# Kernel tuning notes

Hardware: AMD Instinct MI355X
Metric: run time of the kernel (lower is better)

Reference implementation:

```python
import jax, jax.numpy as jnp
import numpy as np

D_MODEL = 1024
N_HEADS = 16
HEAD_DIM = D_MODEL // N_HEADS  # 64
GRID = 8  # 8x8 Ising grid over head_dim pixels
N_DIFF_STEPS = 2
STEPS_PER_SAMPLE = 8  # cfg sampling.steps_per_sample
BETA_START = 0.8
BETA_END = 1.2


def setup_inputs() -> dict:
    key = jax.random.key(0)
    k1, k2, k3 = jax.random.split(key, 3)
    B, N = 4, 4096
    q = jax.random.normal(k1, (B, N, D_MODEL), dtype=jnp.float32)
    k = jax.random.normal(k2, (B, N, D_MODEL), dtype=jnp.float32)
    v = jax.random.normal(k3, (B, N, D_MODEL), dtype=jnp.float32)
    return {"q": q, "k": k, "v": v}


def _nbr_field(s):
    # s: (..., G, G) spins in {-1, +1}; 4-neighbor sum with open (non-torus) boundary
    zr = jnp.zeros_like(s[..., :1, :])
    zc = jnp.zeros_like(s[..., :, :1])
    up = jnp.concatenate([s[..., 1:, :], zr], axis=-2)
    down = jnp.concatenate([zr, s[..., :-1, :]], axis=-2)
    left = jnp.concatenate([s[..., :, 1:], zc], axis=-1)
    right = jnp.concatenate([zc, s[..., :, :-1]], axis=-1)
    return up + down + left + right


def _fta_forward(v):
    B, N, D = v.shape
    H, HD = N_HEADS, HEAD_DIM
    # binarize values -> Ising spins per head: (B, H, N, G, G)
    vh = v.reshape(B, N, H, HD).transpose(0, 2, 1, 3)
    spins = jnp.where(vh > 0, 1.0, -1.0).astype(jnp.float32).reshape(B, H, N, GRID, GRID)

    # log-spaced beta schedule (diffusion_schedule kind='log'), each diffusion
    # step runs STEPS_PER_SAMPLE Gibbs sweeps
    betas = jnp.exp(jnp.linspace(jnp.log(BETA_START), jnp.log(BETA_END), N_DIFF_STEPS))
    betas = jnp.repeat(betas, STEPS_PER_SAMPLE)  # (T,)
    T = N_DIFF_STEPS * STEPS_PER_SAMPLE

    ii, jj = jnp.meshgrid(jnp.arange(GRID), jnp.arange(GRID), indexing="ij")
    parity = ((ii + jj) % 2).astype(jnp.float32)  # checkerboard mask (G, G)

    keys = jax.random.split(jax.random.key(1234), T)

    def gibbs_step(s, xs):
        beta, kk = xs
        k0, k1 = jax.random.split(kk)

        def half_sweep(s, mask, kh):
            h = _nbr_field(s)
            p = jax.nn.sigmoid(2.0 * beta * h)  # P(spin=+1 | neighbors)
            u = jax.random.uniform(kh, s.shape, dtype=s.dtype)
            new = jnp.where(u < p, 1.0, -1.0)
            return jnp.where(mask > 0.5, new, s)

        s = half_sweep(s, parity, k0)
        s = half_sweep(s, 1.0 - parity, k1)
        return s, None

    spins, _ = jax.lax.scan(gibbs_step, spins, (betas, keys))

    # back to (B, N, D); spins already in {-1, +1} == bool*2-1
    out = spins.reshape(B, H, N, HD).transpose(0, 2, 1, 3).reshape(B, N, D)
    return out


def reference(q, k, v):
    # q and k are accepted for interface fidelity but, as in the source
    # module's head_fta, only v participates in the computation.
    return _fta_forward(v)
```

## Files before the change

kernel.cpp:

```cpp
#include <hip/hip_runtime.h>
#include <stdint.h>
#include <string.h>
#include <math.h>


struct FtaParams {
  uint32_t hk[32][2];
  uint32_t K9[2][9];
};

static inline void tf2x32_host(uint32_t k0, uint32_t k1, uint32_t c0, uint32_t c1,
                               uint32_t& o0, uint32_t& o1) {
  uint32_t ks2 = k0 ^ k1 ^ 0x1BD11BDAu;
  uint32_t x0 = c0 + k0, x1 = c1 + k1;
#define TFR(r) { x0 += x1; x1 = (x1 << (r)) | (x1 >> (32 - (r))); x1 ^= x0; }
  TFR(13) TFR(15) TFR(26) TFR(6)
  x0 += k1;  x1 += ks2 + 1u;
  TFR(17) TFR(29) TFR(16) TFR(24)
  x0 += ks2; x1 += k0 + 2u;
  TFR(13) TFR(15) TFR(26) TFR(6)
  x0 += k0;  x1 += k1 + 3u;
  TFR(17) TFR(29) TFR(16) TFR(24)
  x0 += k1;  x1 += ks2 + 4u;
  TFR(13) TFR(15) TFR(26) TFR(6)
  x0 += ks2; x1 += k0 + 5u;
#undef TFR
  o0 = x0; o1 = x1;
}

__device__ __forceinline__ static void tf_bits4(
    uint32_t K0, uint32_t K1, uint32_t ks2,
    uint32_t i1, uint32_t i2, uint32_t i3, uint32_t i4, uint32_t i5,
    uint32_t m0, uint32_t m1, uint32_t m2, uint32_t m3,
    uint32_t& o0, uint32_t& o1, uint32_t& o2, uint32_t& o3) {
#define ROTL(x, r) __builtin_amdgcn_alignbit((x), (x), 32u - (r))
#define QR4(r)                                                             \
  a0 += a1; b0 += b1; c0 += c1; d0 += d1;                                  \
  a1 = ROTL(a1, r) ^ a0; b1 = ROTL(b1, r) ^ b0;                            \
  c1 = ROTL(c1, r) ^ c0; d1 = ROTL(d1, r) ^ d0;
#define INJ4(sx, si)                                                       \
  a0 += sx; b0 += sx; c0 += sx; d0 += sx;                                  \
  a1 += si; b1 += si; c1 += si; d1 += si;
  uint32_t a1 = m0, b1 = m1, c1 = m2, d1 = m3;
  uint32_t a0 = K0 + a1, b0 = K0 + b1, c0 = K0 + c1, d0 = K0 + d1;
  a1 = ROTL(a1, 13) ^ a0; b1 = ROTL(b1, 13) ^ b0;
  c1 = ROTL(c1, 13) ^ c0; d1 = ROTL(d1, 13) ^ d0;
  QR4(15) QR4(26) QR4(6)
  INJ4(K1, i1)
  QR4(17) QR4(29) QR4(16) QR4(24)
  INJ4(ks2, i2)
  QR4(13) QR4(15) QR4(26) QR4(6)
  INJ4(K0, i3)
  QR4(17) QR4(29) QR4(16) QR4(24)
  INJ4(K1, i4)
  QR4(13) QR4(15) QR4(26) QR4(6)
  a0 += ks2; b0 += ks2; c0 += ks2; d0 += ks2;
  a1 += i5;  b1 += i5;  c1 += i5;  d1 += i5;
  o0 = a0 ^ a1; o1 = b0 ^ b1; o2 = c0 ^ c1; o3 = d0 ^ d1;
#undef QR4
#undef INJ4
#undef ROTL
}

__global__ __launch_bounds__(256, 4) void fta_kernel(const float* __restrict__ v,
                                                     float* __restrict__ out,
                                                     FtaParams P) {
  uint32_t tid = blockIdx.x * 256u + threadIdx.x;
  uint32_t b = tid >> 16;
  uint32_t h = (tid >> 12) & 15u;
  uint32_t n = tid & 4095u;

  size_t voff = ((size_t)(b * 4096u + n)) * 1024u + (size_t)h * 64u;

  uint64_t bd = 0;
#pragma unroll
  for (int k = 0; k < 64; k += 4) {
    float4 a = *reinterpret_cast<const float4*>(v + voff + k);
    bd |= ((uint64_t)(a.x > 0.0f)) << (k + 0);
    bd |= ((uint64_t)(a.y > 0.0f)) << (k + 1);
    bd |= ((uint64_t)(a.z > 0.0f)) << (k + 2);
    bd |= ((uint64_t)(a.w > 0.0f)) << (k + 3);
  }

  uint32_t mbase = tid * 64u;

  uint32_t K[9];
#pragma unroll
  for (int q = 0; q < 9; ++q) K[q] = P.K9[0][q];

  const uint64_t PMASK[2] = { 0x55AA55AA55AA55AAull, 0xAA55AA55AA55AA55ull };

  for (int t = 0; t < 16; ++t) {
    if (t == 8) {
#pragma unroll
      for (int q = 0; q < 9; ++q) K[q] = P.K9[1][q];
    }
#pragma unroll
    for (int hf = 0; hf < 2; ++hf) {
      const uint32_t K0 = P.hk[2 * t + hf][0];
      const uint32_t K1 = P.hk[2 * t + hf][1];
      const uint32_t ks2 = K0 ^ K1 ^ 0x1BD11BDAu;
      const uint32_t i1 = ks2 + 1u, i2 = K0 + 2u, i3 = K1 + 3u,
                     i4 = ks2 + 4u, i5 = K0 + 5u;

      uint64_t U = bd >> 8;
      uint64_t D = bd << 8;
      uint64_t L = (bd >> 1) & 0x7f7f7f7f7f7f7f7full;
      uint64_t R = (bd << 1) & 0xfefefefefefefefeull;
      uint64_t t0 = U ^ D, ca = U & D;
      uint64_t t1 = L ^ R, cb = L & R;
      uint64_t c0 = t0 ^ t1, cc = t0 & t1;
      uint64_t cx = ca ^ cb;
      uint64_t c1 = cx ^ cc;
      uint64_t c2 = (ca & cb) | (cc & cx);

      uint32_t accLo = 0u, accHi = 0u;
#pragma unroll
      for (int i = 0; i < 8; ++i) {
        const int j0 = (i + 1 + hf) & 1;
        const int kr = i * 8 + j0;
        uint32_t bits[4];
        tf_bits4(K0, K1, ks2, i1, i2, i3, i4, i5,
                 mbase + (K1 + (uint32_t)(kr + 0)),
                 mbase + (K1 + (uint32_t)(kr + 2)),
                 mbase + (K1 + (uint32_t)(kr + 4)),
                 mbase + (K1 + (uint32_t)(kr + 6)),
                 bits[0], bits[1], bits[2], bits[3]);
#pragma unroll
        for (int jj = 0; jj < 4; ++jj) {
          const int j = 2 * jj + j0;
          const int k = i * 8 + j;
          uint32_t b0 = (uint32_t)(c0 >> k) & 1u;
          uint32_t b1 = (uint32_t)(c1 >> k) & 1u;
          const int e = (int)(i == 0) + (int)(i == 7) + (int)(j == 0) + (int)(j == 7);
          uint32_t thr;
          if (e == 0) {
            uint32_t b2 = (uint32_t)(c2 >> k) & 1u;
            uint32_t tA = b0 ? K[2] : K[0];
            uint32_t tB = b0 ? K[6] : K[4];
            uint32_t tC = b1 ? tB : tA;
            thr = b2 ? K[8] : tC;
          } else if (e == 1) {
            uint32_t tA = b0 ? K[3] : K[1];
            uint32_t tB = b0 ? K[7] : K[5];
            thr = b1 ? tB : tA;
          } else {
            uint32_t tA = b0 ? K[4] : K[2];
            thr = b1 ? K[6] : tA;
          }

          uint32_t nb = (bits[jj] < thr) ? 1u : 0u;
          if (k < 32) accLo |= nb << k;
          else        accHi |= nb << (k - 32);
        }
      }
      uint64_t acc = ((uint64_t)accHi << 32) | (uint64_t)accLo;
      bd = (bd & ~PMASK[hf]) | acc;
    }
  }

#pragma unroll
  for (int k = 0; k < 64; k += 4) {
    float4 o;
    o.x = ((bd >> (k + 0)) & 1ull) ? 1.0f : -1.0f;
    o.y = ((bd >> (k + 1)) & 1ull) ? 1.0f : -1.0f;
    o.z = ((bd >> (k + 2)) & 1ull) ? 1.0f : -1.0f;
    o.w = ((bd >> (k + 3)) & 1ull) ? 1.0f : -1.0f;
    *reinterpret_cast<float4*>(out + voff + k) = o;
  }
}

static float xla_expf(float xin) {
  const float exp_hi = 88.3762626647950f;
  const float exp_lo = -88.3762626647949f;
  const float LOG2EF = 1.44269504088896341f;
  const float C1 = 0.693359375f;
  const float C2 = -2.12194440e-4f;
  const float Pc0 = 1.9875691500E-4f;
  const float Pc1 = 1.3981999507E-3f;
  const float Pc2 = 8.3334519073E-3f;
  const float Pc3 = 4.1665795894E-2f;
  const float Pc4 = 1.6666665459E-1f;
  const float Pc5 = 5.0000001201E-1f;
#define MA(a, b, c) ((a) * (b) + (c))
  float x = xin;
  if (x > exp_hi) x = exp_hi;
  if (x < exp_lo) x = exp_lo;
  float fx = floorf(MA(x, LOG2EF, 0.5f));
  float tmp = C1 * fx;
  float z = C2 * fx;
  x = x - tmp;
  x = x - z;
  z = x * x;
  float y = MA(x, Pc0, Pc1);
  y = MA(y, x, Pc2);
  y = MA(y, x, Pc3);
  y = MA(y, x, Pc4);
  y = MA(y, x, Pc5);
  y = MA(y, z, x);
  y = y + 1.0f;
  int nn = (int)fx;
  uint32_t eb = (uint32_t)(nn + 127) << 23;
  float p2n;
  memcpy(&p2n, &eb, 4);
  float r = y * p2n;
  return r > xin ? r : xin;
#undef MA
}

extern "C" void kernel_launch(void* const* d_in, const int* in_sizes, int n_in,
                              void* d_out, int out_size, void* d_ws, size_t ws_size,
                              hipStream_t stream) {
  (void)in_sizes; (void)n_in; (void)d_ws; (void)ws_size; (void)out_size;
  const float* v = (const float*)d_in[2];
  float* out = (float*)d_out;

  FtaParams P;

  const uint32_t rk0 = 0u, rk1 = 1234u;
  uint32_t kt[16][2];
  for (uint32_t t = 0; t < 16; ++t) tf2x32_host(rk0, rk1, 0u, t, kt[t][0], kt[t][1]);
  for (int t = 0; t < 16; ++t) {
    uint32_t a0, a1, b0, b1;
    tf2x32_host(kt[t][0], kt[t][1], 0u, 0u, a0, a1);
    tf2x32_host(kt[t][0], kt[t][1], 0u, 1u, b0, b1);
    P.hk[2 * t + 0][0] = a0; P.hk[2 * t + 0][1] = a1;
    P.hk[2 * t + 1][0] = b0; P.hk[2 * t + 1][1] = b1;
  }

  float bet[2];
  bet[0] = (float)exp((double)(float)log((double)0.8f));
  bet[1] = (float)exp((double)(float)log((double)1.2f));

  for (int s = 0; s < 2; ++s) {
    float x2b = 2.0f * bet[s];
    for (int hh = -4; hh <= 4; ++hh) {
      float xh = x2b * (float)hh;
      float e = xla_expf(-xh);
      float p = 1.0f / (1.0f + e);
      double pd = (double)p * 8388608.0;
      uint64_t kc = (uint64_t)ceil(pd);
      uint64_t k9 = kc << 9;
      P.K9[s][hh + 4] = (k9 > 0xFFFFFFFFull) ? 0xFFFFFFFFu : (uint32_t)k9;
    }
  }

  fta_kernel<<<dim3(1024), dim3(256), 0, stream>>>(v, out, P);
}
```

Before: 537.4 us.

## Split each 8x8 Ising grid across two lanes exchanging boundary rows via shuffle

```diff
diff --git a/kernel.cpp b/kernel.cpp
--- a/kernel.cpp
+++ b/kernel.cpp
@@ -62,33 +62,39 @@
 #undef ROTL
 }
 
-__global__ __launch_bounds__(256, 4) void fta_kernel(const float* __restrict__ v,
+__global__ __launch_bounds__(256, 8) void fta_kernel(const float* __restrict__ v,
                                                      float* __restrict__ out,
                                                      FtaParams P) {
   uint32_t tid = blockIdx.x * 256u + threadIdx.x;
-  uint32_t b = tid >> 16;
-  uint32_t h = (tid >> 12) & 15u;
-  uint32_t n = tid & 4095u;
-
-  size_t voff = ((size_t)(b * 4096u + n)) * 1024u + (size_t)h * 64u;
-
-  uint64_t bd = 0;
-#pragma unroll
-  for (int k = 0; k < 64; k += 4) {
+  const int half = (int)(tid & 1u);
+  uint32_t g = tid >> 1;
+  uint32_t b = g >> 16;
+  uint32_t h = (g >> 12) & 15u;
+  uint32_t n = g & 4095u;
+
+  size_t voff = ((size_t)(b * 4096u + n)) * 1024u + (size_t)h * 64u
+              + (size_t)(half * 32);
+
+  uint32_t nat = 0u;
+#pragma unroll
+  for (int k = 0; k < 32; k += 4) {
     float4 a = *reinterpret_cast<const float4*>(v + voff + k);
-    bd |= ((uint64_t)(a.x > 0.0f)) << (k + 0);
-    bd |= ((uint64_t)(a.y > 0.0f)) << (k + 1);
-    bd |= ((uint64_t)(a.z > 0.0f)) << (k + 2);
-    bd |= ((uint64_t)(a.w > 0.0f)) << (k + 3);
-  }
-
-  uint32_t mbase = tid * 64u;
+    nat |= ((uint32_t)(a.x > 0.0f)) << (k + 0);
+    nat |= ((uint32_t)(a.y > 0.0f)) << (k + 1);
+    nat |= ((uint32_t)(a.z > 0.0f)) << (k + 2);
+    nat |= ((uint32_t)(a.w > 0.0f)) << (k + 3);
+  }
+  uint32_t bd = half ? __brev(nat) : nat;
+
+  const uint32_t mgrid = g * 64u;
+  const uint32_t mpc = mgrid + (half ? 63u : 0u);
+  const int sgn = half ? -1 : 1;
 
   uint32_t K[9];
 #pragma unroll
   for (int q = 0; q < 9; ++q) K[q] = P.K9[0][q];
 
-  const uint64_t PMASK[2] = { 0x55AA55AA55AA55AAull, 0xAA55AA55AA55AA55ull };
+  const uint32_t PM[2] = { 0x55AA55AAu, 0xAA55AA55u };
 
   for (int t = 0; t < 16; ++t) {
     if (t == 8) {
@@ -102,70 +108,73 @@
       const uint32_t ks2 = K0 ^ K1 ^ 0x1BD11BDAu;
       const uint32_t i1 = ks2 + 1u, i2 = K0 + 2u, i3 = K1 + 3u,
                      i4 = ks2 + 4u, i5 = K0 + 5u;
-
-      uint64_t U = bd >> 8;
-      uint64_t D = bd << 8;
-      uint64_t L = (bd >> 1) & 0x7f7f7f7f7f7f7f7full;
-      uint64_t R = (bd << 1) & 0xfefefefefefefefeull;
-      uint64_t t0 = U ^ D, ca = U & D;
-      uint64_t t1 = L ^ R, cb = L & R;
-      uint64_t c0 = t0 ^ t1, cc = t0 & t1;
-      uint64_t cx = ca ^ cb;
-      uint64_t c1 = cx ^ cc;
-      uint64_t c2 = (ca & cb) | (cc & cx);
-
-      uint32_t accLo = 0u, accHi = 0u;
-#pragma unroll
-      for (int i = 0; i < 8; ++i) {
-        const int j0 = (i + 1 + hf) & 1;
-        const int kr = i * 8 + j0;
+      const uint32_t cKp = mpc + K1;
+
+      uint32_t myrow3 = bd >> 24;
+      uint32_t xrow = (uint32_t)__shfl_xor((int)myrow3, 1, 64);
+      uint32_t xb = __brev(xrow) >> 24;
+
+      uint32_t U  = (bd >> 8) | (xb << 24);
+      uint32_t D  = bd << 8;
+      uint32_t Lp = (bd >> 1) & 0x7f7f7f7fu;
+      uint32_t Rp = (bd << 1) & 0xfefefefeu;
+      uint32_t t0 = U ^ D,  ca = U & D;
+      uint32_t t1 = Lp ^ Rp, cb = Lp & Rp;
+      uint32_t c0 = t0 ^ t1, cc = t0 & t1;
+      uint32_t cx = ca ^ cb;
+      uint32_t c1 = cx ^ cc;
+      uint32_t c2 = (ca & cb) | (cc & cx);
+
+      uint32_t acc = 0u;
+#pragma unroll
+      for (int lr = 0; lr < 4; ++lr) {
+        const int j0 = (lr + 1 + hf) & 1;
+        const int L0 = lr * 8 + j0;
         uint32_t bits[4];
         tf_bits4(K0, K1, ks2, i1, i2, i3, i4, i5,
-                 mbase + (K1 + (uint32_t)(kr + 0)),
-                 mbase + (K1 + (uint32_t)(kr + 2)),
-                 mbase + (K1 + (uint32_t)(kr + 4)),
-                 mbase + (K1 + (uint32_t)(kr + 6)),
+                 (uint32_t)((int)cKp + sgn * (L0 + 0)),
+                 (uint32_t)((int)cKp + sgn * (L0 + 2)),
+                 (uint32_t)((int)cKp + sgn * (L0 + 4)),
+                 (uint32_t)((int)cKp + sgn * (L0 + 6)),
                  bits[0], bits[1], bits[2], bits[3]);
 #pragma unroll
         for (int jj = 0; jj < 4; ++jj) {
-          const int j = 2 * jj + j0;
-          const int k = i * 8 + j;
-          uint32_t b0 = (uint32_t)(c0 >> k) & 1u;
-          uint32_t b1 = (uint32_t)(c1 >> k) & 1u;
-          const int e = (int)(i == 0) + (int)(i == 7) + (int)(j == 0) + (int)(j == 7);
+          const int lc = j0 + 2 * jj;
+          const int L = lr * 8 + lc;
+          uint32_t b0v = (c0 >> L) & 1u;
+          uint32_t b1v = (c1 >> L) & 1u;
+          const int e = (int)(lr == 0) + (int)(lc == 0) + (int)(lc == 7);
           uint32_t thr;
           if (e == 0) {
-            uint32_t b2 = (uint32_t)(c2 >> k) & 1u;
-            uint32_t tA = b0 ? K[2] : K[0];
-            uint32_t tB = b0 ? K[6] : K[4];
-            uint32_t tC = b1 ? tB : tA;
-            thr = b2 ? K[8] : tC;
+            uint32_t b2v = (c2 >> L) & 1u;
+            uint32_t tA = b0v ? K[2] : K[0];
+            uint32_t tB = b0v ? K[6] : K[4];
+            uint32_t tC = b1v ? tB : tA;
+            thr = b2v ? K[8] : tC;
           } else if (e == 1) {
-            uint32_t tA = b0 ? K[3] : K[1];
-            uint32_t tB = b0 ? K[7] : K[5];
-            thr = b1 ? tB : tA;
+            uint32_t tA = b0v ? K[3] : K[1];
+            uint32_t tB = b0v ? K[7] : K[5];
+            thr = b1v ? tB : tA;
           } else {
-            uint32_t tA = b0 ? K[4] : K[2];
-            thr = b1 ? K[6] : tA;
+            uint32_t tA = b0v ? K[4] : K[2];
+            thr = b1v ? K[6] : tA;
           }
-
           uint32_t nb = (bits[jj] < thr) ? 1u : 0u;
-          if (k < 32) accLo |= nb << k;
-          else        accHi |= nb << (k - 32);
+          acc |= nb << L;
         }
       }
-      uint64_t acc = ((uint64_t)accHi << 32) | (uint64_t)accLo;
-      bd = (bd & ~PMASK[hf]) | acc;
+      bd = (bd & ~PM[hf]) | acc;
     }
   }
 
-#pragma unroll
-  for (int k = 0; k < 64; k += 4) {
+  uint32_t nato = half ? __brev(bd) : bd;
+#pragma unroll
+  for (int k = 0; k < 32; k += 4) {
     float4 o;
-    o.x = ((bd >> (k + 0)) & 1ull) ? 1.0f : -1.0f;
-    o.y = ((bd >> (k + 1)) & 1ull) ? 1.0f : -1.0f;
-    o.z = ((bd >> (k + 2)) & 1ull) ? 1.0f : -1.0f;
-    o.w = ((bd >> (k + 3)) & 1ull) ? 1.0f : -1.0f;
+    o.x = ((nato >> (k + 0)) & 1u) ? 1.0f : -1.0f;
+    o.y = ((nato >> (k + 1)) & 1u) ? 1.0f : -1.0f;
+    o.z = ((nato >> (k + 2)) & 1u) ? 1.0f : -1.0f;
+    o.w = ((nato >> (k + 3)) & 1u) ? 1.0f : -1.0f;
     *reinterpret_cast<float4*>(out + voff + k) = o;
   }
 }
@@ -245,5 +254,5 @@
     }
   }
 
-  fta_kernel<<<dim3(1024), dim3(256), 0, stream>>>(v, out, P);
-}
+  fta_kernel<<<dim3(2048), dim3(256), 0, stream>>>(v, out, P);
+}
```

Measured after the change: 529.8 us. About the same (-1.4%).
